# Kernel optimization log

Measured on AMD Instinct MI355X. Metric: run time of the kernel, lower is better.

Reference implementation:

```python
import jax, jax.numpy as jnp
import numpy as np

B, S, D, H, FF, E = 2, 2048, 1024, 16, 4096, 8
HD = D // H

def setup_inputs() -> dict:
    key = jax.random.key(0)
    ks = jax.random.split(key, 8)
    s = lambda k, shape: jax.random.normal(k, shape, jnp.float32) * 0.02
    return dict(
        x=jax.random.normal(ks[0], (B, S, D), jnp.float32),
        in_proj_w=s(ks[1], (3 * D, D)), in_proj_b=jnp.zeros((3 * D,), jnp.float32),
        out_proj_w=s(ks[2], (D, D)), out_proj_b=jnp.zeros((D,), jnp.float32),
        ln1_g=jnp.ones((D,), jnp.float32), ln1_b=jnp.zeros((D,), jnp.float32),
        ln2_g=jnp.ones((D,), jnp.float32), ln2_b=jnp.zeros((D,), jnp.float32),
        gate_w=s(ks[3], (E, D)), gate_b=jnp.zeros((E,), jnp.float32),
        w1=s(ks[4], (E, FF, D)), b1=jnp.zeros((E, FF), jnp.float32),
        w2=s(ks[5], (E, D, FF)), b2=jnp.zeros((E, D), jnp.float32),
    )

def _layer_norm(x, g, b, eps=1e-5):
    mu = x.mean(-1, keepdims=True)
    var = ((x - mu) ** 2).mean(-1, keepdims=True)
    return (x - mu) * jax.lax.rsqrt(var + eps) * g + b

def _mha(x, wqkv, bqkv, wo, bo):
    qkv = x @ wqkv.T + bqkv                      # [B,S,3D]
    q, k, v = jnp.split(qkv, 3, axis=-1)
    rs = lambda t: t.reshape(B, S, H, HD).transpose(0, 2, 1, 3)  # [B,H,S,HD]
    q, k, v = rs(q), rs(k), rs(v)
    scale = jnp.asarray(1.0 / np.sqrt(HD), jnp.float32)
    att = jax.nn.softmax(jnp.einsum('bhqd,bhkd->bhqk', q, k) * scale, axis=-1)
    o = jnp.einsum('bhqk,bhkd->bhqd', att, v).transpose(0, 2, 1, 3).reshape(B, S, D)
    return o @ wo.T + bo

def _moe(x, gw, gb, w1, b1, w2, b2):
    xt = x.reshape(-1, D)                        # [T,D]
    # NaiveGate, top_k=1: softmax over a single selected logit -> combine weight 1.0
    idx = jnp.argmax(xt @ gw.T + gb, axis=-1)    # [T]
    y = jnp.zeros_like(xt)
    for e in range(E):                           # fixed small loop over experts
        m = (idx == e).astype(xt.dtype)[:, None]
        h = jax.nn.gelu((xt * m) @ w1[e].T + b1[e], approximate=False)
        y = y + m * (h @ w2[e].T + b2[e])
    return y.reshape(x.shape)

def reference(x, in_proj_w, in_proj_b, out_proj_w, out_proj_b,
              ln1_g, ln1_b, ln2_g, ln2_b, gate_w, gate_b, w1, b1, w2, b2):
    x = _layer_norm(x + _mha(x, in_proj_w, in_proj_b, out_proj_w, out_proj_b), ln1_g, ln1_b)
    x = _layer_norm(x + _moe(x, gate_w, gate_b, w1, b1, w2, b2), ln2_g, ln2_b)
    return x
```

## Files before the change

kernel.cpp:

```cpp
#include <hip/hip_runtime.h>
#include <hip/hip_bf16.h>

typedef __bf16 bf16;
typedef __attribute__((ext_vector_type(8))) __bf16 bf16x8;
typedef __attribute__((ext_vector_type(4))) float f32x4;

#define NB 2
#define NS 2048
#define ND 1024
#define NH 16
#define NHD 64
#define NFF 4096
#define NE 8
#define NT 4096

typedef const void __attribute__((address_space(1)))* gas_p;
typedef void __attribute__((address_space(3)))* las_p;

__device__ __forceinline__ void gload16(const bf16* g, char* l) {
  __builtin_amdgcn_global_load_lds((gas_p)g, (las_p)l, 16, 0, 0);
}

__device__ __forceinline__ float bf2f(bf16 v) { return (float)v; }

__global__ void cvt_kernel(const float* __restrict__ in, bf16* __restrict__ out, int n)
{
  for (int i = (blockIdx.x * 256 + threadIdx.x) * 8; i < n; i += gridDim.x * 256 * 8) {
    float4 a = *(const float4*)(in + i);
    float4 b = *(const float4*)(in + i + 4);
    bf16x8 o;
    o[0] = (bf16)a.x; o[1] = (bf16)a.y; o[2] = (bf16)a.z; o[3] = (bf16)a.w;
    o[4] = (bf16)b.x; o[5] = (bf16)b.y; o[6] = (bf16)b.z; o[7] = (bf16)b.w;
    *(bf16x8*)(out + i) = o;
  }
}

template<int MODE>
__launch_bounds__(256, 2)
__global__ void gemm_bt(const bf16* __restrict__ A, const bf16* __restrict__ Bw,
                        const float* __restrict__ bias, const float* __restrict__ residf,
                        float* __restrict__ outf,
                        bf16* __restrict__ qws, bf16* __restrict__ kws, bf16* __restrict__ vtws,
                        int M, int N, int K)
{
  __shared__ __align__(16) char smem[32768];
  char* smemA = smem;
  char* smemB = smem + 16384;
  const int tid = threadIdx.x;
  const int lane = tid & 63, w = tid >> 6;
  const int wr = w >> 1, wc = w & 1;
  const int l4 = lane >> 4, l15 = lane & 15;
  const int m0 = blockIdx.x * 128, n0 = blockIdx.y * 128;

  const bf16* arow[4];
  const bf16* brow[4];
  int ldsoff[4];
#pragma unroll
  for (int it = 0; it < 4; ++it) {
    int chunk = it * 256 + tid;
    int row = chunk >> 3, p = chunk & 7;
    int xoff = (p ^ (row & 7)) * 8;
    ldsoff[it] = chunk * 16;
    arow[it] = A + (size_t)(m0 + row) * K + xoff;
    brow[it] = Bw + (size_t)(n0 + row) * K + xoff;
  }

  f32x4 acc[4][4];
  const f32x4 z4 = {0.f, 0.f, 0.f, 0.f};
#pragma unroll
  for (int i = 0; i < 4; ++i)
#pragma unroll
    for (int j = 0; j < 4; ++j) acc[i][j] = z4;

  for (int kt = 0; kt < K; kt += 64) {
    __syncthreads();
#pragma unroll
    for (int it = 0; it < 4; ++it) {
      gload16(arow[it] + kt, smemA + ldsoff[it]);
      gload16(brow[it] + kt, smemB + ldsoff[it]);
    }
    __syncthreads();
#pragma unroll
    for (int ks = 0; ks < 2; ++ks) {
      bf16x8 af[4], bfr[4];
#pragma unroll
      for (int i = 0; i < 4; ++i) {
        int r = wr * 64 + i * 16 + l15;
        int ps = (ks * 4 + l4) ^ (r & 7);
        af[i] = *(const bf16x8*)(smemA + r * 128 + ps * 16);
      }
#pragma unroll
      for (int j = 0; j < 4; ++j) {
        int r = wc * 64 + j * 16 + l15;
        int ps = (ks * 4 + l4) ^ (r & 7);
        bfr[j] = *(const bf16x8*)(smemB + r * 128 + ps * 16);
      }
#pragma unroll
      for (int i = 0; i < 4; ++i)
#pragma unroll
        for (int j = 0; j < 4; ++j)
          acc[i][j] = __builtin_amdgcn_mfma_f32_16x16x32_bf16(af[i], bfr[j], acc[i][j], 0, 0, 0);
    }
  }

#pragma unroll
  for (int i = 0; i < 4; ++i) {
#pragma unroll
    for (int j = 0; j < 4; ++j) {
      int col = n0 + wc * 64 + j * 16 + l15;
      float bv = bias[col];
#pragma unroll
      for (int r = 0; r < 4; ++r) {
        int rl = wr * 64 + i * 16 + l4 * 4 + r;
        int grow = m0 + rl;
        float val = acc[i][j][r] + bv;
        if (MODE == 0) {
          int b = grow >> 11, s = grow & 2047;
          int which = col >> 10, d = col & 1023;
          int h = d >> 6, hd = d & 63;
          int bh = b * NH + h;
          if (which == 0)      qws[((size_t)(bh * NS + s)) * NHD + hd] = (bf16)val;
          else if (which == 1) kws[((size_t)(bh * NS + s)) * NHD + hd] = (bf16)val;
          else                 vtws[((size_t)(bh * NHD + hd)) * NS + s] = (bf16)val;
        } else {
          size_t o = (size_t)grow * ND + col;
          outf[o] = val + residf[o];
        }
      }
    }
  }
}

template<int MODE, int BM, int MINW>
__launch_bounds__(256, MINW)
__global__ void gemm_moe(const bf16* __restrict__ A, const bf16* __restrict__ Bw,
                         const float* __restrict__ bias, const bf16* __restrict__ residb,
                         float* __restrict__ outf, bf16* __restrict__ outb,
                         const int* __restrict__ perm, const int* __restrict__ offs,
                         const int* __restrict__ tiles, int NTILN, int K)
{
  constexpr int BN = 128;
  constexpr int AI = BM / 32;
  constexpr int BI = 4;
  constexpr int STRIDE = (BM + BN) * 128;
  constexpr int WM = 2, WN = 2;
  constexpr int IM = BM / (16 * WM);
  constexpr int JN = BN / (16 * WN);
  __shared__ __align__(16) char smem[2 * STRIDE];
  const int tid = threadIdx.x;
  const int lane = tid & 63, w = tid >> 6;
  const int wr = w >> 1, wc = w & 1;
  const int l4 = lane >> 4, l15 = lane & 15;

  const int nmt = tiles[0];
  const int ntile = nmt * NTILN;
  const int q8 = ntile >> 3, r8 = ntile & 7;
  const int NSTEP = K >> 6;

  for (int u = blockIdx.x; u < ntile; u += gridDim.x) {
    const int xcd = u & 7, pos = u >> 3;
    const int t = (xcd < r8 ? xcd * (q8 + 1) : r8 * (q8 + 1) + (xcd - r8) * q8) + pos;

    const int mi = t % nmt, nj = t / nmt;
    const int pk = tiles[1 + mi];
    const int z = pk >> 16;
    const int m0 = (pk & 0xffff) * BM;
    const int n0 = nj * BN;
    const int slot0 = offs[z];
    const int ne = offs[z + 1] - slot0;
    const bf16* Bp = Bw + (size_t)z * ((MODE == 2) ? (NFF * ND) : (ND * NFF));
    const float* biasp = bias + z * ((MODE == 2) ? NFF : ND);

    const bf16* arow[AI];
    const bf16* brow[BI];
    int aoff[AI], boff[BI];
#pragma unroll
    for (int it = 0; it < AI; ++it) {
      int chunk = it * 256 + tid;
      int row = chunk >> 3, p = chunk & 7;
      int xoff = (p ^ (row & 7)) * 8;
      aoff[it] = chunk * 16;
      if (MODE == 2) {
        int tok = perm[slot0 + min(m0 + row, ne - 1)];
        arow[it] = A + (size_t)tok * K + xoff;
      } else {
        int r2 = min(m0 + row, ne - 1);
        arow[it] = A + (size_t)(slot0 + r2) * K + xoff;
      }
    }
#pragma unroll
    for (int it = 0; it < BI; ++it) {
      int chunk = it * 256 + tid;
      int row = chunk >> 3, p = chunk & 7;
      int xoff = (p ^ (row & 7)) * 8;
      boff[it] = BM * 128 + chunk * 16;
      brow[it] = Bp + (size_t)(n0 + row) * K + xoff;
    }

    f32x4 acc[IM][JN];
    const f32x4 z4 = {0.f, 0.f, 0.f, 0.f};
#pragma unroll
    for (int i = 0; i < IM; ++i)
#pragma unroll
      for (int j = 0; j < JN; ++j) acc[i][j] = z4;

#pragma unroll
    for (int it = 0; it < AI; ++it) gload16(arow[it], smem + aoff[it]);
#pragma unroll
    for (int it = 0; it < BI; ++it) gload16(brow[it], smem + boff[it]);
#pragma unroll
    for (int it = 0; it < AI; ++it) gload16(arow[it] + 64, smem + STRIDE + aoff[it]);
#pragma unroll
    for (int it = 0; it < BI; ++it) gload16(brow[it] + 64, smem + STRIDE + boff[it]);
    asm volatile("s_waitcnt vmcnt(6)" ::: "memory");
    __builtin_amdgcn_sched_barrier(0);
    __builtin_amdgcn_s_barrier();

    int cur = 0;
    for (int st = 0; st < NSTEP; ++st) {
      const char* sA = smem + cur * STRIDE;
      const char* sB = sA + BM * 128;
#pragma unroll
      for (int ks = 0; ks < 2; ++ks) {
        bf16x8 af[IM], bfr[JN];
#pragma unroll
        for (int i = 0; i < IM; ++i) {
          int r = wr * 16 * IM + i * 16 + l15;
          int ps = (ks * 4 + l4) ^ (r & 7);
          af[i] = *(const bf16x8*)(sA + r * 128 + ps * 16);
        }
#pragma unroll
        for (int j = 0; j < JN; ++j) {
          int r = wc * 16 * JN + j * 16 + l15;
          int ps = (ks * 4 + l4) ^ (r & 7);
          bfr[j] = *(const bf16x8*)(sB + r * 128 + ps * 16);
        }
#pragma unroll
        for (int i = 0; i < IM; ++i)
#pragma unroll
          for (int j = 0; j < JN; ++j)
            acc[i][j] = __builtin_amdgcn_mfma_f32_16x16x32_bf16(af[i], bfr[j], acc[i][j], 0, 0, 0);
      }
      __builtin_amdgcn_s_barrier();
      if (st + 2 < NSTEP) {
        const int kt2 = (st + 2) << 6;
#pragma unroll
        for (int it = 0; it < AI; ++it) gload16(arow[it] + kt2, smem + cur * STRIDE + aoff[it]);
#pragma unroll
        for (int it = 0; it < BI; ++it) gload16(brow[it] + kt2, smem + cur * STRIDE + boff[it]);
        asm volatile("s_waitcnt vmcnt(6)" ::: "memory");
      } else {
        asm volatile("s_waitcnt vmcnt(0)" ::: "memory");
      }
      __builtin_amdgcn_sched_barrier(0);
      __builtin_amdgcn_s_barrier();
      cur ^= 1;
    }

#pragma unroll
    for (int i = 0; i < IM; ++i) {
#pragma unroll
      for (int j = 0; j < JN; ++j) {
        int col = n0 + wc * 16 * JN + j * 16 + l15;
        float bv = biasp[col];
#pragma unroll
        for (int r = 0; r < 4; ++r) {
          int rl = wr * 16 * IM + i * 16 + l4 * 4 + r;
          int grow = m0 + rl;
          if (grow < ne) {
            float val = acc[i][j][r] + bv;
            if (MODE == 2) {
              size_t o = ((size_t)(slot0 + grow)) * NFF + col;
              float c = val * (val * val * 0.044715f + 1.0f) * 0.7978845608f;
              float e = __expf(2.0f * c);
              float gl = 0.5f * val * (1.0f + (e - 1.0f) / (e + 1.0f));
              outb[o] = (bf16)gl;
            } else {
              int tok = perm[slot0 + grow];
              size_t o = (size_t)tok * ND + col;
              outf[o] = val + bf2f(residb[o]);
            }
          }
        }
      }
    }
  }
}

__launch_bounds__(256, 4)
__global__ void attn_kernel(const bf16* __restrict__ qws, const bf16* __restrict__ kws,
                            const bf16* __restrict__ vtws, bf16* __restrict__ attn_out,
                            const float* __restrict__ w1f, const float* __restrict__ w2f,
                            bf16* __restrict__ bw1, bf16* __restrict__ bw2)
{
  const int tid = threadIdx.x, lane = tid & 63, w = tid >> 6;
  const int l4 = lane >> 4, l15 = lane & 15;
  const int bh = blockIdx.y, q0 = blockIdx.x * 64 + w * 16;
  const bf16* Qb = qws + ((size_t)bh * NS + q0) * NHD;
  const bf16* Kb = kws + (size_t)bh * NS * NHD;
  const bf16* Vb = vtws + (size_t)bh * NHD * NS;

  const int fb = blockIdx.y * 32 + blockIdx.x;
  const float* cvsrc;
  bf16* cvdst;
  size_t cbase;
  if (fb < 512) { cvsrc = w1f; cvdst = bw1; cbase = (size_t)fb * 65536; }
  else          { cvsrc = w2f; cvdst = bw2; cbase = (size_t)(fb - 512) * 65536; }

  __shared__ __align__(16) char sK[8192];
  __shared__ __align__(16) char sV[8192];
  __shared__ __align__(16) bf16 sP[4][16][64];

  const int c0 = tid, c1 = 256 + tid;
  const int r0 = c0 >> 3, x0 = ((c0 & 7) ^ (r0 & 7)) * 8;
  const int r1 = c1 >> 3, x1 = ((c1 & 7) ^ (r1 & 7)) * 8;
  const bf16* kst0 = Kb + r0 * NHD + x0;
  const bf16* kst1 = Kb + r1 * NHD + x1;
  const bf16* vst0 = Vb + (size_t)r0 * NS + x0;
  const bf16* vst1 = Vb + (size_t)r1 * NS + x1;
  char* dK0 = sK + tid * 16;        char* dK1 = sK + 4096 + tid * 16;
  char* dV0 = sV + tid * 16;        char* dV1 = sV + 4096 + tid * 16;

  bf16x8 qa[2];
#pragma unroll
  for (int ks = 0; ks < 2; ++ks)
    qa[ks] = *(const bf16x8*)(Qb + (size_t)l15 * NHD + ks * 32 + l4 * 8);

  const f32x4 z4 = {0.f, 0.f, 0.f, 0.f};
  f32x4 o[4];
  float srun[4];
#pragma unroll
  for (int j = 0; j < 4; ++j) o[j] = z4;
#pragma unroll
  for (int r = 0; r < 4; ++r) srun[r] = 0.f;

  for (int t = 0; t < 32; ++t) {
    __syncthreads();
    gload16(kst0 + t * 4096, dK0);
    gload16(kst1 + t * 4096, dK1);
    gload16(vst0 + t * 64, dV0);
    gload16(vst1 + t * 64, dV1);
    __syncthreads();

    const size_t coff = cbase + (size_t)(t * 256 + tid) * 8;
    float4 ca = *(const float4*)(cvsrc + coff);
    float4 cb = *(const float4*)(cvsrc + coff + 4);

    f32x4 s[4];
#pragma unroll
    for (int j = 0; j < 4; ++j) s[j] = z4;
#pragma unroll
    for (int ks = 0; ks < 2; ++ks) {
      bf16x8 kf[4];
#pragma unroll
      for (int j = 0; j < 4; ++j) {
        int r = j * 16 + l15;
        int ps = (ks * 4 + l4) ^ (r & 7);
        kf[j] = *(const bf16x8*)(sK + r * 128 + ps * 16);
      }
#pragma unroll
      for (int j = 0; j < 4; ++j)
        s[j] = __builtin_amdgcn_mfma_f32_16x16x32_bf16(qa[ks], kf[j], s[j], 0, 0, 0);
    }
#pragma unroll
    for (int r = 0; r < 4; ++r) {
      const int row = l4 * 4 + r;
      float ps = 0.f;
#pragma unroll
      for (int j = 0; j < 4; ++j) {
        float p = __expf(s[j][r] * 0.125f);
        int col = j * 16 + l15;
        int slot = (col >> 3) ^ (row & 7);
        sP[w][row][slot * 8 + (col & 7)] = (bf16)p;
        ps += p;
      }
      srun[r] += ps;
    }
#pragma unroll
    for (int ks2 = 0; ks2 < 2; ++ks2) {
      int slot = (ks2 * 4 + l4) ^ (l15 & 7);
      bf16x8 pa = *(const bf16x8*)&sP[w][l15][slot * 8];
      bf16x8 vf[4];
#pragma unroll
      for (int j = 0; j < 4; ++j) {
        int r = j * 16 + l15;
        int ps2 = (ks2 * 4 + l4) ^ (r & 7);
        vf[j] = *(const bf16x8*)(sV + r * 128 + ps2 * 16);
      }
#pragma unroll
      for (int j = 0; j < 4; ++j)
        o[j] = __builtin_amdgcn_mfma_f32_16x16x32_bf16(pa, vf[j], o[j], 0, 0, 0);
    }

    bf16x8 co;
    co[0] = (bf16)ca.x; co[1] = (bf16)ca.y; co[2] = (bf16)ca.z; co[3] = (bf16)ca.w;
    co[4] = (bf16)cb.x; co[5] = (bf16)cb.y; co[6] = (bf16)cb.z; co[7] = (bf16)cb.w;
    *(bf16x8*)(cvdst + coff) = co;
  }

#pragma unroll
  for (int r = 0; r < 4; ++r) {
    float s = srun[r];
    s += __shfl_xor(s, 1); s += __shfl_xor(s, 2);
    s += __shfl_xor(s, 4); s += __shfl_xor(s, 8);
    srun[r] = 1.f / s;
  }
  const int b = bh >> 4, h = bh & 15;
#pragma unroll
  for (int j = 0; j < 4; ++j)
#pragma unroll
    for (int r = 0; r < 4; ++r) {
      int q = q0 + l4 * 4 + r;
      float v = o[j][r] * srun[r];
      attn_out[((size_t)(b * NS + q)) * ND + h * NHD + j * 16 + l15] = (bf16)v;
    }
}

template<int OUTF>
__global__ void ln_kernel(const float* __restrict__ in, const float* __restrict__ g,
                          const float* __restrict__ b, void* __restrict__ outp)
{
  const int t = blockIdx.x, tid = threadIdx.x;
  const float4 xv = ((const float4*)(in + (size_t)t * ND))[tid];
  __shared__ float red[8];
  float s = xv.x + xv.y + xv.z + xv.w;
  s += __shfl_xor(s, 32); s += __shfl_xor(s, 16); s += __shfl_xor(s, 8);
  s += __shfl_xor(s, 4);  s += __shfl_xor(s, 2);  s += __shfl_xor(s, 1);
  if ((tid & 63) == 0) red[tid >> 6] = s;
  __syncthreads();
  const float mean = (red[0] + red[1] + red[2] + red[3]) * (1.f / 1024.f);
  float d0 = xv.x - mean, d1 = xv.y - mean, d2 = xv.z - mean, d3 = xv.w - mean;
  float v = d0 * d0 + d1 * d1 + d2 * d2 + d3 * d3;
  v += __shfl_xor(v, 32); v += __shfl_xor(v, 16); v += __shfl_xor(v, 8);
  v += __shfl_xor(v, 4);  v += __shfl_xor(v, 2);  v += __shfl_xor(v, 1);
  if ((tid & 63) == 0) red[4 + (tid >> 6)] = v;
  __syncthreads();
  const float var = (red[4] + red[5] + red[6] + red[7]) * (1.f / 1024.f);
  const float rstd = rsqrtf(var + 1e-5f);
  const float4 gv = ((const float4*)g)[tid];
  const float4 bv = ((const float4*)b)[tid];
  float o0 = d0 * rstd * gv.x + bv.x;
  float o1 = d1 * rstd * gv.y + bv.y;
  float o2 = d2 * rstd * gv.z + bv.z;
  float o3 = d3 * rstd * gv.w + bv.w;
  if (OUTF) {
    float4 ov = {o0, o1, o2, o3};
    ((float4*)((float*)outp + (size_t)t * ND))[tid] = ov;
  } else {
    unsigned short u0 = __builtin_bit_cast(unsigned short, (bf16)o0);
    unsigned short u1 = __builtin_bit_cast(unsigned short, (bf16)o1);
    unsigned short u2 = __builtin_bit_cast(unsigned short, (bf16)o2);
    unsigned short u3 = __builtin_bit_cast(unsigned short, (bf16)o3);
    uint2 pk;
    pk.x = (unsigned)u0 | ((unsigned)u1 << 16);
    pk.y = (unsigned)u2 | ((unsigned)u3 << 16);
    ((uint2*)((bf16*)outp + (size_t)t * ND))[tid] = pk;
  }
}

__global__ void gate_kernel(const float* __restrict__ x1, const float* __restrict__ ln1g,
                            const float* __restrict__ ln1b, const float* __restrict__ gw,
                            const float* __restrict__ gb, int* __restrict__ idx,
                            int* __restrict__ counts)
{
  const int token = blockIdx.x * 4 + (threadIdx.x >> 6);
  const int lane = threadIdx.x & 63;
  const float* xp = x1 + (size_t)token * ND + lane * 16;
  float xr[16];
#pragma unroll
  for (int q = 0; q < 4; ++q) {
    float4 t = *(const float4*)(xp + q * 4);
    xr[q * 4 + 0] = t.x; xr[q * 4 + 1] = t.y; xr[q * 4 + 2] = t.z; xr[q * 4 + 3] = t.w;
  }
  float s = 0.f;
#pragma unroll
  for (int q = 0; q < 16; ++q) s += xr[q];
  s += __shfl_xor(s, 32); s += __shfl_xor(s, 16); s += __shfl_xor(s, 8);
  s += __shfl_xor(s, 4);  s += __shfl_xor(s, 2);  s += __shfl_xor(s, 1);
  const float mean = s * (1.f / 1024.f);
  float v = 0.f;
#pragma unroll
  for (int q = 0; q < 16; ++q) { float d = xr[q] - mean; v += d * d; }
  v += __shfl_xor(v, 32); v += __shfl_xor(v, 16); v += __shfl_xor(v, 8);
  v += __shfl_xor(v, 4);  v += __shfl_xor(v, 2);  v += __shfl_xor(v, 1);
  const float rstd = rsqrtf(v * (1.f / 1024.f) + 1e-5f);
  float xln[16];
#pragma unroll
  for (int q = 0; q < 4; ++q) {
    float4 gv = *(const float4*)(ln1g + lane * 16 + q * 4);
    float4 bv = *(const float4*)(ln1b + lane * 16 + q * 4);
    xln[q * 4 + 0] = (xr[q * 4 + 0] - mean) * rstd * gv.x + bv.x;
    xln[q * 4 + 1] = (xr[q * 4 + 1] - mean) * rstd * gv.y + bv.y;
    xln[q * 4 + 2] = (xr[q * 4 + 2] - mean) * rstd * gv.z + bv.z;
    xln[q * 4 + 3] = (xr[q * 4 + 3] - mean) * rstd * gv.w + bv.w;
  }
  float acc[NE];
#pragma unroll
  for (int e = 0; e < NE; ++e) {
    const float* gp = gw + (size_t)e * ND + lane * 16;
    float a = 0.f;
#pragma unroll
    for (int q = 0; q < 4; ++q) {
      float4 t = *(const float4*)(gp + q * 4);
      a += xln[q * 4 + 0] * t.x + xln[q * 4 + 1] * t.y + xln[q * 4 + 2] * t.z + xln[q * 4 + 3] * t.w;
    }
    acc[e] = a;
  }
#pragma unroll
  for (int e = 0; e < NE; ++e) {
    acc[e] += __shfl_xor(acc[e], 32); acc[e] += __shfl_xor(acc[e], 16);
    acc[e] += __shfl_xor(acc[e], 8);  acc[e] += __shfl_xor(acc[e], 4);
    acc[e] += __shfl_xor(acc[e], 2);  acc[e] += __shfl_xor(acc[e], 1);
  }
  if (lane == 0) {
    int best = 0;
    float bvv = acc[0] + gb[0];
#pragma unroll
    for (int e = 1; e < NE; ++e) {
      float vv = acc[e] + gb[e];
      if (vv > bvv) { bvv = vv; best = e; }
    }
    idx[token] = best;
    atomicAdd(&counts[best], 1);
  }
}

__global__ void zero_meta(int* p) { if (threadIdx.x < 32) p[threadIdx.x] = 0; }

__global__ void plan_kernel(const int* __restrict__ counts, int* __restrict__ offs,
                            int* __restrict__ tiles1, int* __restrict__ tiles2)
{
  if (threadIdx.x != 0) return;
  int o = 0, n1 = 0, n2 = 0;
  for (int e = 0; e < NE; ++e) {
    offs[e] = o;
    int ne = counts[e];
    int nm = (ne + 63) >> 6;
    for (int m = 0; m < nm; ++m) {
      tiles1[1 + n1++] = (e << 16) | m;
      tiles2[1 + n2++] = (e << 16) | m;
    }
    o += ne;
  }
  offs[NE] = o;
  tiles1[0] = n1;
  tiles2[0] = n2;
}

__global__ void scatter_kernel(const int* __restrict__ idx, const int* __restrict__ offs,
                               int* __restrict__ cursor, int* __restrict__ perm)
{
  int t = blockIdx.x * 256 + threadIdx.x;
  int e = idx[t];
  int pos = offs[e] + atomicAdd(&cursor[e], 1);
  perm[pos] = t;
}

extern "C" void kernel_launch(void* const* d_in, const int* in_sizes, int n_in,
                              void* d_out, int out_size, void* d_ws, size_t ws_size,
                              hipStream_t stream)
{
  (void)in_sizes; (void)n_in; (void)out_size; (void)ws_size;
  const float* x    = (const float*)d_in[0];
  const float* wqkv = (const float*)d_in[1];
  const float* bqkv = (const float*)d_in[2];
  const float* wo   = (const float*)d_in[3];
  const float* bo   = (const float*)d_in[4];
  const float* ln1g = (const float*)d_in[5];
  const float* ln1b = (const float*)d_in[6];
  const float* ln2g = (const float*)d_in[7];
  const float* ln2b = (const float*)d_in[8];
  const float* gw   = (const float*)d_in[9];
  const float* gb   = (const float*)d_in[10];
  const float* w1   = (const float*)d_in[11];
  const float* b1   = (const float*)d_in[12];
  const float* w2   = (const float*)d_in[13];
  const float* b2   = (const float*)d_in[14];
  float* out = (float*)d_out;

  char* ws = (char*)d_ws;
  bf16*  bx    = (bf16*)(ws + 0);
  bf16*  bwqkv = (bf16*)(ws + 8388608);
  bf16*  bwo   = (bf16*)(ws + 14680064);
  bf16*  bw1   = (bf16*)(ws + 16777216);
  bf16*  bw2   = (bf16*)(ws + 83886080);
  bf16*  qws   = (bf16*)(ws + 150994944);
  bf16*  kws   = (bf16*)(ws + 159383552);
  bf16*  vtws  = (bf16*)(ws + 167772160);
  bf16*  aout  = (bf16*)(ws + 176160768);
  bf16*  hbuf  = (bf16*)(ws + 150994944);
  float* x1    = (float*)(ws + 184549376);
  float* x2    = (float*)(ws + 184549376);
  bf16*  u     = (bf16*)(ws + 201326592);
  int*   meta  = (int*)(ws + 209715200);
  int* idx    = meta;
  int* perm   = meta + 4096;
  int* counts = meta + 8192;
  int* cursor = meta + 8200;
  int* offs   = meta + 8208;
  int* tiles1 = meta + 8224;
  int* tiles2 = meta + 8320;

  cvt_kernel<<<2048, 256, 0, stream>>>(x, bx, NT * ND);
  cvt_kernel<<<1536, 256, 0, stream>>>(wqkv, bwqkv, 3 * ND * ND);
  cvt_kernel<<<512, 256, 0, stream>>>(wo, bwo, ND * ND);

  gemm_bt<0><<<dim3(32, 24), 256, 0, stream>>>(bx, bwqkv, bqkv, nullptr, nullptr,
                                               qws, kws, vtws, NT, 3 * ND, ND);
  attn_kernel<<<dim3(32, 32), 256, 0, stream>>>(qws, kws, vtws, aout,
                                                w1, w2, bw1, bw2);
  gemm_bt<1><<<dim3(32, 8), 256, 0, stream>>>(aout, bwo, bo, x, x1,
                                              nullptr, nullptr, nullptr, NT, ND, ND);
  ln_kernel<0><<<4096, 256, 0, stream>>>(x1, ln1g, ln1b, u);
  zero_meta<<<1, 32, 0, stream>>>(counts);
  gate_kernel<<<1024, 256, 0, stream>>>(x1, ln1g, ln1b, gw, gb, idx, counts);
  plan_kernel<<<1, 64, 0, stream>>>(counts, offs, tiles1, tiles2);
  scatter_kernel<<<16, 256, 0, stream>>>(idx, offs, cursor, perm);
  gemm_moe<2, 64, 3><<<768, 256, 0, stream>>>(u, bw1, b1, nullptr, nullptr, hbuf,
                                              perm, offs, tiles1, NFF / 128, ND);
  gemm_moe<3, 64, 3><<<576, 256, 0, stream>>>(hbuf, bw2, b2, u, x2, nullptr,
                                              perm, offs, tiles2, ND / 128, NFF);
  ln_kernel<1><<<4096, 256, 0, stream>>>(x2, ln2g, ln2b, out);
}
```

Measured before the change: 436.1 us.

## Double-buffer LDS tiles in GEMM and attention with two-stage async prefetch

```diff
diff --git a/kernel.cpp b/kernel.cpp
--- a/kernel.cpp
+++ b/kernel.cpp
@@ -43,9 +43,8 @@
                         bf16* __restrict__ qws, bf16* __restrict__ kws, bf16* __restrict__ vtws,
                         int M, int N, int K)
 {
-  __shared__ __align__(16) char smem[32768];
-  char* smemA = smem;
-  char* smemB = smem + 16384;
+  constexpr int STRIDE = 32768;
+  __shared__ __align__(16) char smem[2 * STRIDE];
   const int tid = threadIdx.x;
   const int lane = tid & 63, w = tid >> 6;
   const int wr = w >> 1, wc = w & 1;
@@ -54,13 +53,14 @@
 
   const bf16* arow[4];
   const bf16* brow[4];
-  int ldsoff[4];
+  int aoff[4], boff[4];
 #pragma unroll
   for (int it = 0; it < 4; ++it) {
     int chunk = it * 256 + tid;
     int row = chunk >> 3, p = chunk & 7;
     int xoff = (p ^ (row & 7)) * 8;
-    ldsoff[it] = chunk * 16;
+    aoff[it] = chunk * 16;
+    boff[it] = 16384 + chunk * 16;
     arow[it] = A + (size_t)(m0 + row) * K + xoff;
     brow[it] = Bw + (size_t)(n0 + row) * K + xoff;
   }
@@ -72,14 +72,21 @@
 #pragma unroll
     for (int j = 0; j < 4; ++j) acc[i][j] = z4;
 
-  for (int kt = 0; kt < K; kt += 64) {
-    __syncthreads();
-#pragma unroll
-    for (int it = 0; it < 4; ++it) {
-      gload16(arow[it] + kt, smemA + ldsoff[it]);
-      gload16(brow[it] + kt, smemB + ldsoff[it]);
-    }
-    __syncthreads();
+  const int NSTEP = K >> 6;
+#pragma unroll
+  for (int it = 0; it < 4; ++it) { gload16(arow[it], smem + aoff[it]);
+                                   gload16(brow[it], smem + boff[it]); }
+#pragma unroll
+  for (int it = 0; it < 4; ++it) { gload16(arow[it] + 64, smem + STRIDE + aoff[it]);
+                                   gload16(brow[it] + 64, smem + STRIDE + boff[it]); }
+  asm volatile("s_waitcnt vmcnt(8)" ::: "memory");
+  __builtin_amdgcn_sched_barrier(0);
+  __builtin_amdgcn_s_barrier();
+
+  int cur = 0;
+  for (int st = 0; st < NSTEP; ++st) {
+    const char* sA = smem + cur * STRIDE;
+    const char* sB = sA + 16384;
 #pragma unroll
     for (int ks = 0; ks < 2; ++ks) {
       bf16x8 af[4], bfr[4];
@@ -87,13 +94,13 @@
       for (int i = 0; i < 4; ++i) {
         int r = wr * 64 + i * 16 + l15;
         int ps = (ks * 4 + l4) ^ (r & 7);
-        af[i] = *(const bf16x8*)(smemA + r * 128 + ps * 16);
+        af[i] = *(const bf16x8*)(sA + r * 128 + ps * 16);
       }
 #pragma unroll
       for (int j = 0; j < 4; ++j) {
         int r = wc * 64 + j * 16 + l15;
         int ps = (ks * 4 + l4) ^ (r & 7);
-        bfr[j] = *(const bf16x8*)(smemB + r * 128 + ps * 16);
+        bfr[j] = *(const bf16x8*)(sB + r * 128 + ps * 16);
       }
 #pragma unroll
       for (int i = 0; i < 4; ++i)
@@ -101,6 +108,19 @@
         for (int j = 0; j < 4; ++j)
           acc[i][j] = __builtin_amdgcn_mfma_f32_16x16x32_bf16(af[i], bfr[j], acc[i][j], 0, 0, 0);
     }
+    __builtin_amdgcn_s_barrier();
+    if (st + 2 < NSTEP) {
+      const int kt2 = (st + 2) << 6;
+#pragma unroll
+      for (int it = 0; it < 4; ++it) { gload16(arow[it] + kt2, smem + cur * STRIDE + aoff[it]);
+                                       gload16(brow[it] + kt2, smem + cur * STRIDE + boff[it]); }
+      asm volatile("s_waitcnt vmcnt(8)" ::: "memory");
+    } else {
+      asm volatile("s_waitcnt vmcnt(0)" ::: "memory");
+    }
+    __builtin_amdgcn_sched_barrier(0);
+    __builtin_amdgcn_s_barrier();
+    cur ^= 1;
   }
 
 #pragma unroll
@@ -307,8 +327,7 @@
   if (fb < 512) { cvsrc = w1f; cvdst = bw1; cbase = (size_t)fb * 65536; }
   else          { cvsrc = w2f; cvdst = bw2; cbase = (size_t)(fb - 512) * 65536; }
 
-  __shared__ __align__(16) char sK[8192];
-  __shared__ __align__(16) char sV[8192];
+  __shared__ __align__(16) char sbuf[2][16384];
   __shared__ __align__(16) bf16 sP[4][16][64];
 
   const int c0 = tid, c1 = 256 + tid;
@@ -318,8 +337,6 @@
   const bf16* kst1 = Kb + r1 * NHD + x1;
   const bf16* vst0 = Vb + (size_t)r0 * NS + x0;
   const bf16* vst1 = Vb + (size_t)r1 * NS + x1;
-  char* dK0 = sK + tid * 16;        char* dK1 = sK + 4096 + tid * 16;
-  char* dV0 = sV + tid * 16;        char* dV1 = sV + 4096 + tid * 16;
 
   bf16x8 qa[2];
 #pragma unroll
@@ -334,13 +351,25 @@
 #pragma unroll
   for (int r = 0; r < 4; ++r) srun[r] = 0.f;
 
+  {
+    char* b0 = sbuf[0]; char* b1 = sbuf[1];
+    gload16(kst0, b0 + tid * 16);
+    gload16(kst1, b0 + 4096 + tid * 16);
+    gload16(vst0, b0 + 8192 + tid * 16);
+    gload16(vst1, b0 + 12288 + tid * 16);
+    gload16(kst0 + 4096, b1 + tid * 16);
+    gload16(kst1 + 4096, b1 + 4096 + tid * 16);
+    gload16(vst0 + 64, b1 + 8192 + tid * 16);
+    gload16(vst1 + 64, b1 + 12288 + tid * 16);
+  }
+  asm volatile("s_waitcnt vmcnt(4)" ::: "memory");
+  __builtin_amdgcn_sched_barrier(0);
+  __builtin_amdgcn_s_barrier();
+
   for (int t = 0; t < 32; ++t) {
-    __syncthreads();
-    gload16(kst0 + t * 4096, dK0);
-    gload16(kst1 + t * 4096, dK1);
-    gload16(vst0 + t * 64, dV0);
-    gload16(vst1 + t * 64, dV1);
-    __syncthreads();
+    const int cur = t & 1;
+    const char* sK = sbuf[cur];
+    const char* sV = sbuf[cur] + 8192;
 
     const size_t coff = cbase + (size_t)(t * 256 + tid) * 8;
     float4 ca = *(const float4*)(cvsrc + coff);
@@ -396,6 +425,23 @@
     co[0] = (bf16)ca.x; co[1] = (bf16)ca.y; co[2] = (bf16)ca.z; co[3] = (bf16)ca.w;
     co[4] = (bf16)cb.x; co[5] = (bf16)cb.y; co[6] = (bf16)cb.z; co[7] = (bf16)cb.w;
     *(bf16x8*)(cvdst + coff) = co;
+
+    if (t + 2 < 32) {
+      __builtin_amdgcn_s_barrier();
+      char* bd = sbuf[cur];
+      gload16(kst0 + (t + 2) * 4096, bd + tid * 16);
+      gload16(kst1 + (t + 2) * 4096, bd + 4096 + tid * 16);
+      gload16(vst0 + (t + 2) * 64, bd + 8192 + tid * 16);
+      gload16(vst1 + (t + 2) * 64, bd + 12288 + tid * 16);
+      asm volatile("s_waitcnt vmcnt(6)" ::: "memory");
+      __builtin_amdgcn_sched_barrier(0);
+      __builtin_amdgcn_s_barrier();
+    } else if (t + 1 < 32) {
+      __builtin_amdgcn_s_barrier();
+      asm volatile("s_waitcnt vmcnt(2)" ::: "memory");
+      __builtin_amdgcn_sched_barrier(0);
+      __builtin_amdgcn_s_barrier();
+    }
   }
 
 #pragma unroll
```

Result: no change. 438.2 us (+0.5%).

## Double-buffer dense GEMM LDS loads and fuse LN1 with gating

Applied to the files above, without the earlier changes.

```diff
diff --git a/kernel.cpp b/kernel.cpp
--- a/kernel.cpp
+++ b/kernel.cpp
@@ -23,8 +23,10 @@
 
 __device__ __forceinline__ float bf2f(bf16 v) { return (float)v; }
 
-__global__ void cvt_kernel(const float* __restrict__ in, bf16* __restrict__ out, int n)
-{
+__global__ void cvt_kernel(const float* __restrict__ in, bf16* __restrict__ out,
+                           int n, int* __restrict__ mz)
+{
+  if (mz && blockIdx.x == 0 && threadIdx.x < 32) mz[threadIdx.x] = 0;
   for (int i = (blockIdx.x * 256 + threadIdx.x) * 8; i < n; i += gridDim.x * 256 * 8) {
     float4 a = *(const float4*)(in + i);
     float4 b = *(const float4*)(in + i + 4);
@@ -43,9 +45,8 @@
                         bf16* __restrict__ qws, bf16* __restrict__ kws, bf16* __restrict__ vtws,
                         int M, int N, int K)
 {
-  __shared__ __align__(16) char smem[32768];
-  char* smemA = smem;
-  char* smemB = smem + 16384;
+  constexpr int STRIDE = 32768;
+  __shared__ __align__(16) char smem[2 * STRIDE];
   const int tid = threadIdx.x;
   const int lane = tid & 63, w = tid >> 6;
   const int wr = w >> 1, wc = w & 1;
@@ -54,13 +55,14 @@
 
   const bf16* arow[4];
   const bf16* brow[4];
-  int ldsoff[4];
+  int aoff[4], boff[4];
 #pragma unroll
   for (int it = 0; it < 4; ++it) {
     int chunk = it * 256 + tid;
     int row = chunk >> 3, p = chunk & 7;
     int xoff = (p ^ (row & 7)) * 8;
-    ldsoff[it] = chunk * 16;
+    aoff[it] = chunk * 16;
+    boff[it] = 16384 + chunk * 16;
     arow[it] = A + (size_t)(m0 + row) * K + xoff;
     brow[it] = Bw + (size_t)(n0 + row) * K + xoff;
   }
@@ -72,14 +74,21 @@
 #pragma unroll
     for (int j = 0; j < 4; ++j) acc[i][j] = z4;
 
-  for (int kt = 0; kt < K; kt += 64) {
-    __syncthreads();
-#pragma unroll
-    for (int it = 0; it < 4; ++it) {
-      gload16(arow[it] + kt, smemA + ldsoff[it]);
-      gload16(brow[it] + kt, smemB + ldsoff[it]);
-    }
-    __syncthreads();
+  const int NSTEP = K >> 6;
+#pragma unroll
+  for (int it = 0; it < 4; ++it) { gload16(arow[it], smem + aoff[it]);
+                                   gload16(brow[it], smem + boff[it]); }
+#pragma unroll
+  for (int it = 0; it < 4; ++it) { gload16(arow[it] + 64, smem + STRIDE + aoff[it]);
+                                   gload16(brow[it] + 64, smem + STRIDE + boff[it]); }
+  asm volatile("s_waitcnt vmcnt(8)" ::: "memory");
+  __builtin_amdgcn_sched_barrier(0);
+  __builtin_amdgcn_s_barrier();
+
+  int cur = 0;
+  for (int st = 0; st < NSTEP; ++st) {
+    const char* sA = smem + cur * STRIDE;
+    const char* sB = sA + 16384;
 #pragma unroll
     for (int ks = 0; ks < 2; ++ks) {
       bf16x8 af[4], bfr[4];
@@ -87,13 +96,13 @@
       for (int i = 0; i < 4; ++i) {
         int r = wr * 64 + i * 16 + l15;
         int ps = (ks * 4 + l4) ^ (r & 7);
-        af[i] = *(const bf16x8*)(smemA + r * 128 + ps * 16);
+        af[i] = *(const bf16x8*)(sA + r * 128 + ps * 16);
       }
 #pragma unroll
       for (int j = 0; j < 4; ++j) {
         int r = wc * 64 + j * 16 + l15;
         int ps = (ks * 4 + l4) ^ (r & 7);
-        bfr[j] = *(const bf16x8*)(smemB + r * 128 + ps * 16);
+        bfr[j] = *(const bf16x8*)(sB + r * 128 + ps * 16);
       }
 #pragma unroll
       for (int i = 0; i < 4; ++i)
@@ -101,6 +110,19 @@
         for (int j = 0; j < 4; ++j)
           acc[i][j] = __builtin_amdgcn_mfma_f32_16x16x32_bf16(af[i], bfr[j], acc[i][j], 0, 0, 0);
     }
+    __builtin_amdgcn_s_barrier();
+    if (st + 2 < NSTEP) {
+      const int kt2 = (st + 2) << 6;
+#pragma unroll
+      for (int it = 0; it < 4; ++it) { gload16(arow[it] + kt2, smem + cur * STRIDE + aoff[it]);
+                                       gload16(brow[it] + kt2, smem + cur * STRIDE + boff[it]); }
+      asm volatile("s_waitcnt vmcnt(8)" ::: "memory");
+    } else {
+      asm volatile("s_waitcnt vmcnt(0)" ::: "memory");
+    }
+    __builtin_amdgcn_sched_barrier(0);
+    __builtin_amdgcn_s_barrier();
+    cur ^= 1;
   }
 
 #pragma unroll
@@ -416,9 +438,76 @@
     }
 }
 
-template<int OUTF>
-__global__ void ln_kernel(const float* __restrict__ in, const float* __restrict__ g,
-                          const float* __restrict__ b, void* __restrict__ outp)
+__global__ void ln1_gate_kernel(const float* __restrict__ in, const float* __restrict__ g,
+                                const float* __restrict__ b, const float* __restrict__ gw,
+                                const float* __restrict__ gb, bf16* __restrict__ u,
+                                int* __restrict__ idx, int* __restrict__ counts)
+{
+  const int t = blockIdx.x, tid = threadIdx.x;
+  const int lane = tid & 63, w = tid >> 6;
+  const float4 xv = ((const float4*)(in + (size_t)t * ND))[tid];
+  __shared__ float red[8];
+  __shared__ float sG[4][8];
+  float s = xv.x + xv.y + xv.z + xv.w;
+  s += __shfl_xor(s, 32); s += __shfl_xor(s, 16); s += __shfl_xor(s, 8);
+  s += __shfl_xor(s, 4);  s += __shfl_xor(s, 2);  s += __shfl_xor(s, 1);
+  if (lane == 0) red[w] = s;
+  __syncthreads();
+  const float mean = (red[0] + red[1] + red[2] + red[3]) * (1.f / 1024.f);
+  float d0 = xv.x - mean, d1 = xv.y - mean, d2 = xv.z - mean, d3 = xv.w - mean;
+  float v = d0 * d0 + d1 * d1 + d2 * d2 + d3 * d3;
+  v += __shfl_xor(v, 32); v += __shfl_xor(v, 16); v += __shfl_xor(v, 8);
+  v += __shfl_xor(v, 4);  v += __shfl_xor(v, 2);  v += __shfl_xor(v, 1);
+  if (lane == 0) red[4 + w] = v;
+  __syncthreads();
+  const float var = (red[4] + red[5] + red[6] + red[7]) * (1.f / 1024.f);
+  const float rstd = rsqrtf(var + 1e-5f);
+  const float4 gv = ((const float4*)g)[tid];
+  const float4 bv = ((const float4*)b)[tid];
+  const float o0 = d0 * rstd * gv.x + bv.x;
+  const float o1 = d1 * rstd * gv.y + bv.y;
+  const float o2 = d2 * rstd * gv.z + bv.z;
+  const float o3 = d3 * rstd * gv.w + bv.w;
+  unsigned short u0 = __builtin_bit_cast(unsigned short, (bf16)o0);
+  unsigned short u1 = __builtin_bit_cast(unsigned short, (bf16)o1);
+  unsigned short u2 = __builtin_bit_cast(unsigned short, (bf16)o2);
+  unsigned short u3 = __builtin_bit_cast(unsigned short, (bf16)o3);
+  uint2 pk;
+  pk.x = (unsigned)u0 | ((unsigned)u1 << 16);
+  pk.y = (unsigned)u2 | ((unsigned)u3 << 16);
+  ((uint2*)(u + (size_t)t * ND))[tid] = pk;
+
+  float pe[NE];
+#pragma unroll
+  for (int e = 0; e < NE; ++e) {
+    float4 gw4 = ((const float4*)(gw + (size_t)e * ND))[tid];
+    pe[e] = o0 * gw4.x + o1 * gw4.y + o2 * gw4.z + o3 * gw4.w;
+  }
+#pragma unroll
+  for (int e = 0; e < NE; ++e) {
+    pe[e] += __shfl_xor(pe[e], 32); pe[e] += __shfl_xor(pe[e], 16);
+    pe[e] += __shfl_xor(pe[e], 8);  pe[e] += __shfl_xor(pe[e], 4);
+    pe[e] += __shfl_xor(pe[e], 2);  pe[e] += __shfl_xor(pe[e], 1);
+  }
+  if (lane == 0)
+#pragma unroll
+    for (int e = 0; e < NE; ++e) sG[w][e] = pe[e];
+  __syncthreads();
+  if (tid == 0) {
+    int best = 0;
+    float bvv = sG[0][0] + sG[1][0] + sG[2][0] + sG[3][0] + gb[0];
+#pragma unroll
+    for (int e = 1; e < NE; ++e) {
+      float vv = sG[0][e] + sG[1][e] + sG[2][e] + sG[3][e] + gb[e];
+      if (vv > bvv) { bvv = vv; best = e; }
+    }
+    idx[t] = best;
+    atomicAdd(&counts[best], 1);
+  }
+}
+
+__global__ void ln2_kernel(const float* __restrict__ in, const float* __restrict__ g,
+                           const float* __restrict__ b, float* __restrict__ outp)
 {
   const int t = blockIdx.x, tid = threadIdx.x;
   const float4 xv = ((const float4*)(in + (size_t)t * ND))[tid];
@@ -439,93 +528,13 @@
   const float rstd = rsqrtf(var + 1e-5f);
   const float4 gv = ((const float4*)g)[tid];
   const float4 bv = ((const float4*)b)[tid];
-  float o0 = d0 * rstd * gv.x + bv.x;
-  float o1 = d1 * rstd * gv.y + bv.y;
-  float o2 = d2 * rstd * gv.z + bv.z;
-  float o3 = d3 * rstd * gv.w + bv.w;
-  if (OUTF) {
-    float4 ov = {o0, o1, o2, o3};
-    ((float4*)((float*)outp + (size_t)t * ND))[tid] = ov;
-  } else {
-    unsigned short u0 = __builtin_bit_cast(unsigned short, (bf16)o0);
-    unsigned short u1 = __builtin_bit_cast(unsigned short, (bf16)o1);
-    unsigned short u2 = __builtin_bit_cast(unsigned short, (bf16)o2);
-    unsigned short u3 = __builtin_bit_cast(unsigned short, (bf16)o3);
-    uint2 pk;
-    pk.x = (unsigned)u0 | ((unsigned)u1 << 16);
-    pk.y = (unsigned)u2 | ((unsigned)u3 << 16);
-    ((uint2*)((bf16*)outp + (size_t)t * ND))[tid] = pk;
-  }
-}
-
-__global__ void gate_kernel(const float* __restrict__ x1, const float* __restrict__ ln1g,
-                            const float* __restrict__ ln1b, const float* __restrict__ gw,
-                            const float* __restrict__ gb, int* __restrict__ idx,
-                            int* __restrict__ counts)
-{
-  const int token = blockIdx.x * 4 + (threadIdx.x >> 6);
-  const int lane = threadIdx.x & 63;
-  const float* xp = x1 + (size_t)token * ND + lane * 16;
-  float xr[16];
-#pragma unroll
-  for (int q = 0; q < 4; ++q) {
-    float4 t = *(const float4*)(xp + q * 4);
-    xr[q * 4 + 0] = t.x; xr[q * 4 + 1] = t.y; xr[q * 4 + 2] = t.z; xr[q * 4 + 3] = t.w;
-  }
-  float s = 0.f;
-#pragma unroll
-  for (int q = 0; q < 16; ++q) s += xr[q];
-  s += __shfl_xor(s, 32); s += __shfl_xor(s, 16); s += __shfl_xor(s, 8);
-  s += __shfl_xor(s, 4);  s += __shfl_xor(s, 2);  s += __shfl_xor(s, 1);
-  const float mean = s * (1.f / 1024.f);
-  float v = 0.f;
-#pragma unroll
-  for (int q = 0; q < 16; ++q) { float d = xr[q] - mean; v += d * d; }
-  v += __shfl_xor(v, 32); v += __shfl_xor(v, 16); v += __shfl_xor(v, 8);
-  v += __shfl_xor(v, 4);  v += __shfl_xor(v, 2);  v += __shfl_xor(v, 1);
-  const float rstd = rsqrtf(v * (1.f / 1024.f) + 1e-5f);
-  float xln[16];
-#pragma unroll
-  for (int q = 0; q < 4; ++q) {
-    float4 gv = *(const float4*)(ln1g + lane * 16 + q * 4);
-    float4 bv = *(const float4*)(ln1b + lane * 16 + q * 4);
-    xln[q * 4 + 0] = (xr[q * 4 + 0] - mean) * rstd * gv.x + bv.x;
-    xln[q * 4 + 1] = (xr[q * 4 + 1] - mean) * rstd * gv.y + bv.y;
-    xln[q * 4 + 2] = (xr[q * 4 + 2] - mean) * rstd * gv.z + bv.z;
-    xln[q * 4 + 3] = (xr[q * 4 + 3] - mean) * rstd * gv.w + bv.w;
-  }
-  float acc[NE];
-#pragma unroll
-  for (int e = 0; e < NE; ++e) {
-    const float* gp = gw + (size_t)e * ND + lane * 16;
-    float a = 0.f;
-#pragma unroll
-    for (int q = 0; q < 4; ++q) {
-      float4 t = *(const float4*)(gp + q * 4);
-      a += xln[q * 4 + 0] * t.x + xln[q * 4 + 1] * t.y + xln[q * 4 + 2] * t.z + xln[q * 4 + 3] * t.w;
-    }
-    acc[e] = a;
-  }
-#pragma unroll
-  for (int e = 0; e < NE; ++e) {
-    acc[e] += __shfl_xor(acc[e], 32); acc[e] += __shfl_xor(acc[e], 16);
-    acc[e] += __shfl_xor(acc[e], 8);  acc[e] += __shfl_xor(acc[e], 4);
-    acc[e] += __shfl_xor(acc[e], 2);  acc[e] += __shfl_xor(acc[e], 1);
-  }
-  if (lane == 0) {
-    int best = 0;
-    float bvv = acc[0] + gb[0];
-#pragma unroll
-    for (int e = 1; e < NE; ++e) {
-      float vv = acc[e] + gb[e];
-      if (vv > bvv) { bvv = vv; best = e; }
-    }
-    idx[token] = best;
-    atomicAdd(&counts[best], 1);
-  }
-}
-
-__global__ void zero_meta(int* p) { if (threadIdx.x < 32) p[threadIdx.x] = 0; }
+  float4 ov;
+  ov.x = d0 * rstd * gv.x + bv.x;
+  ov.y = d1 * rstd * gv.y + bv.y;
+  ov.z = d2 * rstd * gv.z + bv.z;
+  ov.w = d3 * rstd * gv.w + bv.w;
+  ((float4*)(outp + (size_t)t * ND))[tid] = ov;
+}
 
 __global__ void plan_kernel(const int* __restrict__ counts, int* __restrict__ offs,
                             int* __restrict__ tiles1, int* __restrict__ tiles2)
@@ -601,9 +610,9 @@
   int* tiles1 = meta + 8224;
   int* tiles2 = meta + 8320;
 
-  cvt_kernel<<<2048, 256, 0, stream>>>(x, bx, NT * ND);
-  cvt_kernel<<<1536, 256, 0, stream>>>(wqkv, bwqkv, 3 * ND * ND);
-  cvt_kernel<<<512, 256, 0, stream>>>(wo, bwo, ND * ND);
+  cvt_kernel<<<2048, 256, 0, stream>>>(x, bx, NT * ND, counts);
+  cvt_kernel<<<1536, 256, 0, stream>>>(wqkv, bwqkv, 3 * ND * ND, nullptr);
+  cvt_kernel<<<512, 256, 0, stream>>>(wo, bwo, ND * ND, nullptr);
 
   gemm_bt<0><<<dim3(32, 24), 256, 0, stream>>>(bx, bwqkv, bqkv, nullptr, nullptr,
                                                qws, kws, vtws, NT, 3 * ND, ND);
@@ -611,14 +620,12 @@
                                                 w1, w2, bw1, bw2);
   gemm_bt<1><<<dim3(32, 8), 256, 0, stream>>>(aout, bwo, bo, x, x1,
                                               nullptr, nullptr, nullptr, NT, ND, ND);
-  ln_kernel<0><<<4096, 256, 0, stream>>>(x1, ln1g, ln1b, u);
-  zero_meta<<<1, 32, 0, stream>>>(counts);
-  gate_kernel<<<1024, 256, 0, stream>>>(x1, ln1g, ln1b, gw, gb, idx, counts);
+  ln1_gate_kernel<<<4096, 256, 0, stream>>>(x1, ln1g, ln1b, gw, gb, u, idx, counts);
   plan_kernel<<<1, 64, 0, stream>>>(counts, offs, tiles1, tiles2);
   scatter_kernel<<<16, 256, 0, stream>>>(idx, offs, cursor, perm);
   gemm_moe<2, 64, 3><<<768, 256, 0, stream>>>(u, bw1, b1, nullptr, nullptr, hbuf,
                                               perm, offs, tiles1, NFF / 128, ND);
   gemm_moe<3, 64, 3><<<576, 256, 0, stream>>>(hbuf, bw2, b2, u, x2, nullptr,
                                               perm, offs, tiles2, ND / 128, NFF);
-  ln_kernel<1><<<4096, 256, 0, stream>>>(x2, ln2g, ln2b, out);
-}
+  ln2_kernel<<<4096, 256, 0, stream>>>(x2, ln2g, ln2b, out);
+}
```

After: 416.9 us. 4.4% less time.
